# Optimization experiments

Measured on AMD Instinct MI355X. Metric: run time of the kernel, lower is better.

Reference implementation:

```python
import jax, jax.numpy as jnp
import numpy as np

IMG = 1024
STRIDES = [8, 16, 32, 64, 128]
SIZES = [32, 64, 128, 256, 512]
RATIOS = [0.5, 1.0, 2.0]
MIN_T = 0.4  # config.min_iou_thresh
MAX_T = 0.5  # config.max_iou_thresh (focal loss_type)
B, G = 32, 20  # batch, GT boxes per image (lengths = [20]*32)


def _make_anchors():
    """generate_anchors + get_anchor_shifts: centered anchors on each level's grid."""
    levels = []
    for stride, size in zip(STRIDES, SIZES):
        ws = np.array([size / np.sqrt(r) for r in RATIOS])
        hs = np.array([size * np.sqrt(r) for r in RATIOS])
        base = np.stack([-ws / 2, -hs / 2, ws / 2, hs / 2], axis=1)  # [3,4]
        g = IMG // stride
        xs = (np.arange(g) + 0.5) * stride
        sy, sx = np.meshgrid(xs, xs, indexing='ij')
        shifts = np.stack([sx, sy, sx, sy], axis=-1).reshape(-1, 1, 4)
        levels.append((shifts + base[None]).reshape(-1, 4).astype(np.float32))
    return levels


def setup_inputs() -> dict:
    key = jax.random.key(0)
    k1, k2, k3 = jax.random.split(key, 3)
    ctr = jax.random.uniform(k1, (B, G, 2), minval=64.0, maxval=float(IMG - 64))
    wh = jax.random.uniform(k2, (B, G, 2), minval=16.0, maxval=256.0)
    bb_coord = jnp.concatenate([ctr - 0.5 * wh, ctr + 0.5 * wh], axis=-1)  # [B,G,4] x1y1x2y2
    bird_ids = jax.random.randint(k3, (B, G), 1, 51, dtype=jnp.int32)
    anchors = _make_anchors()
    inp = {'bb_coord': bb_coord, 'bird_ids': bird_ids}
    for i, a in enumerate(anchors):
        inp[f'anchors_l{i}'] = jnp.asarray(a)
    return inp


def _iou(anch, gt):
    a = anch[None, :, None, :]
    g = gt[:, None, :, :]
    iw = jnp.clip(jnp.minimum(a[..., 2], g[..., 2]) - jnp.maximum(a[..., 0], g[..., 0]) + 1.0, 0.0)
    ih = jnp.clip(jnp.minimum(a[..., 3], g[..., 3]) - jnp.maximum(a[..., 1], g[..., 1]) + 1.0, 0.0)
    area_a = (anch[:, 2] - anch[:, 0] + 1.0) * (anch[:, 3] - anch[:, 1] + 1.0)  # [A]
    area_g = (gt[..., 2] - gt[..., 0] + 1.0) * (gt[..., 3] - gt[..., 1] + 1.0)  # [B,G]
    inter = iw * ih
    return inter / (area_a[None, :, None] + area_g[:, None, :] - inter)


def _bbox_transform(ex, gt):
    # ex [A,4] anchors, gt [B,A,4] assigned boxes -> [B,A,4] (dx,dy,dw,dh)
    ew = ex[:, 2] - ex[:, 0] + 1.0
    eh = ex[:, 3] - ex[:, 1] + 1.0
    ecx = ex[:, 0] + 0.5 * ew
    ecy = ex[:, 1] + 0.5 * eh
    gw = gt[..., 2] - gt[..., 0] + 1.0
    gh = gt[..., 3] - gt[..., 1] + 1.0
    gcx = gt[..., 0] + 0.5 * gw
    gcy = gt[..., 1] + 0.5 * gh
    return jnp.stack([(gcx - ecx) / ew, (gcy - ecy) / eh,
                      jnp.log(gw / ew), jnp.log(gh / eh)], axis=-1)


def _assign(bb_coord, bird_ids_f, anchors_list):
    n_lvl = len(anchors_list)
    max_ovs, argmaxs, gt_maxs, gt_args = [], [], [], []
    for anch in anchors_list:
        ov = _iou(anch, bb_coord)                 # [B,A,G]
        max_ovs.append(ov.max(axis=2))            # [B,A]
        argmaxs.append(ov.argmax(axis=2))         # [B,A]
        gt_maxs.append(ov.max(axis=1))            # [B,G]
        gt_args.append(ov.argmax(axis=1))         # [B,G]
    gt_max_level = jnp.stack(gt_maxs, axis=0).argmax(axis=0)  # [B,G]

    labels_out, reg_out = [], []
    brow = jnp.arange(B)[:, None]
    for lvl, anch in enumerate(anchors_list):
        A = anch.shape[0]
        max_ov, amax = max_ovs[lvl], argmaxs[lvl]
        assigned_box = bb_coord[brow, amax]        # [B,A,4]
        assigned_ids = bird_ids_f[brow, amax]      # [B,A]
        # force each GT's best anchor (on its best level) positive
        is_max = gt_max_level == lvl               # [B,G]
        safe_idx = jnp.where(is_max, gt_args[lvl], A)  # OOB -> dropped
        assigned_box = assigned_box.at[brow, safe_idx].set(bb_coord, mode='drop')
        assigned_ids = assigned_ids.at[brow, safe_idx].set(bird_ids_f, mode='drop')
        ignore = (max_ov >= MIN_T) & (max_ov < MAX_T)
        pos = max_ov >= MAX_T
        pos = pos.at[brow, safe_idx].set(True, mode='drop')
        labels = jnp.where(pos, assigned_ids, jnp.where(ignore, -1.0, 0.0))
        reg = jnp.where(pos[..., None], _bbox_transform(anch, assigned_box), 0.0)
        labels_out.append(labels.astype(jnp.int32))
        reg_out.append(reg)
    return jnp.concatenate(labels_out, axis=1), jnp.concatenate(reg_out, axis=1)


def reference(bb_coord, bird_ids, anchors_l0, anchors_l1, anchors_l2, anchors_l3, anchors_l4):
    anchors = [anchors_l0, anchors_l1, anchors_l2, anchors_l3, anchors_l4]
    labels, reg = _assign(bb_coord, bird_ids.astype(jnp.float32), anchors)
    return labels, reg
```

## Files before the change

kernel.cpp:

```cpp
#include <hip/hip_runtime.h>
#include <hip/hip_bf16.h>

#define NB 32
#define NG 20
#define A_TOTAL 65472
#define LAB_OFF ((size_t)NB * A_TOTAL)
#define NSLOT (NB * NG * 5)

__device__ __forceinline__ float b2f(unsigned short u) {
    __hip_bfloat16 h;
    __builtin_memcpy(&h, &u, 2);
    return __bfloat162float(h);
}

__device__ __forceinline__ float4 ldbox(const void* p, int idx, int isbf) {
    if (isbf) {
        const unsigned short* q = (const unsigned short*)p + (size_t)idx * 4;
        return make_float4(b2f(q[0]), b2f(q[1]), b2f(q[2]), b2f(q[3]));
    }
    return ((const float4*)p)[idx];
}

__device__ __forceinline__ int detect_bf(const void* an0) {
    const unsigned short* u = (const unsigned short*)an0;
    return (fabsf(b2f(u[0]) + 18.6274f) < 0.5f &&
            fabsf(b2f(u[2]) - 26.6274f) < 0.5f) ? 1 : 0;
}

__device__ __forceinline__ float decode_id(const void* idsv, int i) {
    unsigned w = ((const unsigned*)idsv)[i];
    return (w <= 50u) ? (float)(int)w : __uint_as_float(w);
}

__device__ __forceinline__ float area1(float4 A) {
#pragma clang fp contract(off)
    return (A.z - A.x + 1.0f) * (A.w - A.y + 1.0f);
}

__device__ __forceinline__ void reg_transform(float4 A, float g0, float g1,
                                              float g2, float g3,
                                              float& t0, float& t1,
                                              float& t2, float& t3) {
#pragma clang fp contract(off)
    const float ew = A.z - A.x + 1.0f, eh = A.w - A.y + 1.0f;
    const float ecx = A.x + 0.5f * ew, ecy = A.y + 0.5f * eh;
    const float gw = g2 - g0 + 1.0f, gh = g3 - g1 + 1.0f;
    const float gcx = g0 + 0.5f * gw, gcy = g1 + 0.5f * gh;
    t0 = (gcx - ecx) / ew;
    t1 = (gcy - ecy) / eh;
    t2 = logf(gw / ew);
    t3 = logf(gh / eh);
}

__device__ __forceinline__ float iou32h(float4 A, float aa,
                                        float4 G, float ag) {
#pragma clang fp contract(off)
    float iw = fminf(A.z, G.z) - fmaxf(A.x, G.x) + 1.0f;
    iw = fmaxf(iw, 0.0f);
    float ih = fminf(A.w, G.w) - fmaxf(A.y, G.y) + 1.0f;
    ih = fmaxf(ih, 0.0f);
    float inter = iw * ih;
    return inter / (aa + ag - inter);
}

__global__ __launch_bounds__(256, 6)
void kCodes(const void* __restrict__ bb, const void* __restrict__ idsv,
            const void* __restrict__ an0, const void* __restrict__ an1,
            const void* __restrict__ an2, const void* __restrict__ an3,
            const void* __restrict__ an4,
            float* __restrict__ out,
            unsigned long long* __restrict__ slots)
{
    __shared__ float4 sbox4[NG];
    __shared__ float  sid[NG];
    __shared__ unsigned long long swk[NG][4];

    const int tid = threadIdx.x;
    const int b = blockIdx.y;
    const int c = blockIdx.x;
    const int isbf = detect_bf(an0);

    if (tid < NG) {
        sbox4[tid] = ldbox(bb, b * NG + tid, isbf);
        sid[tid] = decode_id(idsv, b * NG + tid);
    }
    __syncthreads();

    int l, lbase, count, goff;
    if (c < 48)      { l = 0; lbase = c * 1024;        count = 1024; goff = 0; }
    else if (c < 60) { l = 1; lbase = (c - 48) * 1024; count = 1024; goff = 49152; }
    else if (c < 63) { l = 2; lbase = (c - 60) * 1024; count = 1024; goff = 61440; }
    else if (c == 63){ l = 3; lbase = 0;               count = 768;  goff = 64512; }
    else             { l = 4; lbase = 0;               count = 192;  goff = 65280; }
    const void* an = (l == 0) ? an0 : (l == 1) ? an1
                   : (l == 2) ? an2 : (l == 3) ? an3 : an4;

    float4 A[4];
    float aa[4];
    bool val[4];
#pragma unroll
    for (int k = 0; k < 4; ++k) {
        const int i = tid + k * 256;
        val[k] = (i < count);
        A[k] = val[k] ? ldbox(an, lbase + i, isbf)
                      : make_float4(-1e8f, -1e8f, -1e8f, -1e8f);
        aa[k] = area1(A[k]);
    }

    float mx[4] = {-1.f, -1.f, -1.f, -1.f};
    int mg[4] = {0, 0, 0, 0};
    const int lane = tid & 63;
    const int wave = tid >> 6;

    for (int g = 0; g < NG; ++g) {
        const float4 G = sbox4[g];
        const float ag = area1(G);
        float bvv = -1.0f;
        int bii = 0;
#pragma unroll
        for (int k = 0; k < 4; ++k) {
            const float v = iou32h(A[k], aa[k], G, ag);
            if (v > mx[k]) { mx[k] = v; mg[k] = g; }
            if (v > bvv)   { bvv = v; bii = goff + lbase + tid + k * 256; }
        }
        unsigned long long key =
            ((unsigned long long)__float_as_uint(bvv) << 32)
            | (unsigned)(~(unsigned)bii);
        for (int o = 32; o > 0; o >>= 1) {
            const unsigned long long ok = __shfl_xor(key, o);
            if (ok > key) key = ok;
        }
        if (lane == 0) swk[g][wave] = key;
    }

    float* lab = out + (size_t)b * A_TOTAL;
    float4* rp = (float4*)(out + LAB_OFF) + (size_t)b * A_TOTAL;
#pragma unroll
    for (int k = 0; k < 4; ++k) {
        if (!val[k]) continue;
        const int ga = goff + lbase + tid + k * 256;
        const bool pos = (mx[k] >= 0.5f);
        lab[ga] = pos ? sid[mg[k]] : ((mx[k] >= 0.4f) ? -1.0f : 0.0f);
        float t0 = 0.f, t1 = 0.f, t2 = 0.f, t3 = 0.f;
        if (pos) {
            const float4 G = sbox4[mg[k]];
            reg_transform(A[k], G.x, G.y, G.z, G.w, t0, t1, t2, t3);
        }
        rp[ga] = make_float4(t0, t1, t2, t3);
    }

    __syncthreads();
    if (tid < NG) {
        unsigned long long k0 = swk[tid][0];
        for (int w = 1; w < 4; ++w)
            if (swk[tid][w] > k0) k0 = swk[tid][w];
        atomicMax(&slots[(b * NG + tid) * 5 + l], k0);
    }
}

__global__ __launch_bounds__(64)
void kForce(const void* __restrict__ bb, const void* __restrict__ idsv,
            const void* __restrict__ an0, const void* __restrict__ an1,
            const void* __restrict__ an2, const void* __restrict__ an3,
            const void* __restrict__ an4,
            const unsigned long long* __restrict__ slots,
            float* __restrict__ out)
{
    __shared__ int sforce[NG];
    const int b = blockIdx.x;
    const int g = threadIdx.x;
    const int isbf = detect_bf(an0);

    if (g < NG) {
        const unsigned long long* s = &slots[(b * NG + g) * 5];
        unsigned long long best = s[0];
        for (int l = 1; l < 5; ++l) {
            if ((unsigned)(s[l] >> 32) > (unsigned)(best >> 32)) best = s[l];
        }
        sforce[g] = (int)(~(unsigned)best);
    }
    __syncthreads();

    if (g < NG) {
        const int a = sforce[g];
        bool win = true;
        for (int g2 = g + 1; g2 < NG; ++g2)
            if (sforce[g2] == a) win = false;
        if (win) {
            int l, off;
            if (a < 49152)      { l = 0; off = 0; }
            else if (a < 61440) { l = 1; off = 49152; }
            else if (a < 64512) { l = 2; off = 61440; }
            else if (a < 65280) { l = 3; off = 64512; }
            else                { l = 4; off = 65280; }
            const void* an = (l == 0) ? an0 : (l == 1) ? an1
                           : (l == 2) ? an2 : (l == 3) ? an3 : an4;
            const float4 A = ldbox(an, a - off, isbf);
            const float4 G = ldbox(bb, b * NG + g, isbf);
            out[(size_t)b * A_TOTAL + a] = decode_id(idsv, b * NG + g);
            float t0, t1, t2, t3;
            reg_transform(A, G.x, G.y, G.z, G.w, t0, t1, t2, t3);
            ((float4*)(out + LAB_OFF))[(size_t)b * A_TOTAL + a]
                = make_float4(t0, t1, t2, t3);
        }
    }
}

__global__ __launch_bounds__(1024)
void kFused(const void* __restrict__ bb, const void* __restrict__ idsv,
            const void* __restrict__ an0, const void* __restrict__ an1,
            const void* __restrict__ an2, const void* __restrict__ an3,
            const void* __restrict__ an4,
            float* __restrict__ out)
{
    __shared__ float4 sbox4[NG];
    __shared__ float swv[NG][16];
    __shared__ int   swi[NG][16];
    __shared__ float lvv[NG][5];
    __shared__ int   lvi[NG][5];
    __shared__ float sid[NG];
    __shared__ int   sforce[NG];

    const int tid = threadIdx.x;
    const int b = blockIdx.x;
    const int isbf = detect_bf(an0);

    if (tid < NG) {
        sbox4[tid] = ldbox(bb, b * NG + tid, isbf);
        sid[tid] = decode_id(idsv, b * NG + tid);
    }
    __syncthreads();

    const void* ans[5] = {an0, an1, an2, an3, an4};
    const int lcount[5] = {49152, 12288, 3072, 768, 192};
    const int loffs[5]  = {0, 49152, 61440, 64512, 65280};
    const int lane = tid & 63;
    const int wave = tid >> 6;
    float* myCodes = out + (size_t)b * A_TOTAL;

    for (int l = 0; l < 5; ++l) {
        float bv[NG];
        int bi[NG];
#pragma unroll
        for (int g = 0; g < NG; ++g) { bv[g] = -1.0f; bi[g] = 0x7fffffff; }
        for (int i = tid; i < lcount[l]; i += 1024) {
            const float4 A = ldbox(ans[l], i, isbf);
            const float aa = area1(A);
            float mxv = -1.0f;
            int mgv = 0;
#pragma unroll
            for (int g = 0; g < NG; ++g) {
                const float4 G = sbox4[g];
                const float ag = area1(G);
                float v = iou32h(A, aa, G, ag);
                if (v > mxv) { mxv = v; mgv = g; }
                if (v > bv[g]) { bv[g] = v; bi[g] = i; }
            }
            const int cls = (mxv >= 0.5f) ? 2 : (mxv >= 0.4f) ? 1 : 0;
            myCodes[loffs[l] + i] = (float)(mgv | (cls << 5));
        }
#pragma unroll
        for (int g = 0; g < NG; ++g) {
            float v = bv[g];
            int ix = bi[g];
            for (int o = 32; o > 0; o >>= 1) {
                float ov = __shfl_xor(v, o);
                int   oi = __shfl_xor(ix, o);
                if (ov > v || (ov == v && oi < ix)) { v = ov; ix = oi; }
            }
            if (lane == 0) { swv[g][wave] = v; swi[g][wave] = ix; }
        }
        __syncthreads();
        if (tid < NG) {
            float v = swv[tid][0];
            int ix = swi[tid][0];
            for (int w = 1; w < 16; ++w) {
                float ov = swv[tid][w];
                int   oi = swi[tid][w];
                if (ov > v || (ov == v && oi < ix)) { v = ov; ix = oi; }
            }
            lvv[tid][l] = v;
            lvi[tid][l] = ix;
        }
        __syncthreads();
    }
    if (tid < NG) {
        int bl = 0;
#pragma unroll
        for (int l = 1; l < 5; ++l)
            if (lvv[tid][l] > lvv[tid][bl]) bl = l;
        sforce[tid] = loffs[bl] + lvi[tid][bl];
    }
    __syncthreads();

    float4* rp = (float4*)(out + LAB_OFF);
    for (int a = tid; a < A_TOTAL; a += 1024) {
        int l, off;
        if (a < 49152)      { l = 0; off = 0; }
        else if (a < 61440) { l = 1; off = 49152; }
        else if (a < 64512) { l = 2; off = 61440; }
        else if (a < 65280) { l = 3; off = 64512; }
        else                { l = 4; off = 65280; }
        const int code = (int)myCodes[a];
        const int mgv = code & 31;
        const int cls = code >> 5;
        int fg = -1;
#pragma unroll
        for (int g = 0; g < NG; ++g)
            if (sforce[g] == a) fg = g;
        const bool pos = (cls == 2) || (fg >= 0);
        const int ug = (fg >= 0) ? fg : mgv;
        myCodes[a] = pos ? sid[ug] : ((cls == 1) ? -1.0f : 0.0f);
        float t0 = 0.f, t1 = 0.f, t2 = 0.f, t3 = 0.f;
        if (pos) {
            const float4 A = ldbox(ans[l], a - off, isbf);
            const float4 G = sbox4[ug];
            reg_transform(A, G.x, G.y, G.z, G.w, t0, t1, t2, t3);
        }
        rp[(size_t)b * A_TOTAL + a] = make_float4(t0, t1, t2, t3);
    }
}

extern "C" void kernel_launch(void* const* d_in, const int* in_sizes, int n_in,
                              void* d_out, int out_size, void* d_ws, size_t ws_size,
                              hipStream_t stream) {
    const void* bb = d_in[0];
    const void* ids = d_in[1];
    const void* an[5] = {d_in[2], d_in[3], d_in[4], d_in[5], d_in[6]};
    if (n_in == 7) {
        for (int i = 0; i < 7; ++i) {
            switch (in_sizes[i]) {
                case 2560:   bb    = d_in[i]; break;
                case 640:    ids   = d_in[i]; break;
                case 196608: an[0] = d_in[i]; break;
                case 49152:  an[1] = d_in[i]; break;
                case 12288:  an[2] = d_in[i]; break;
                case 3072:   an[3] = d_in[i]; break;
                case 768:    an[4] = d_in[i]; break;
                default: break;
            }
        }
    }
    float* out = (float*)d_out;
    const size_t need = (size_t)NSLOT * sizeof(unsigned long long);

    if (ws_size >= need) {
        unsigned long long* slots = (unsigned long long*)d_ws;
        (void)hipMemsetAsync(d_ws, 0, need, stream);
        hipLaunchKernelGGL(kCodes, dim3(65, NB), dim3(256), 0, stream,
                           bb, ids, an[0], an[1], an[2], an[3], an[4],
                           out, slots);
        hipLaunchKernelGGL(kForce, dim3(NB), dim3(64), 0, stream,
                           bb, ids, an[0], an[1], an[2], an[3], an[4],
                           slots, out);
    } else {
        hipLaunchKernelGGL(kFused, dim3(NB), dim3(1024), 0, stream,
                           bb, ids, an[0], an[1], an[2], an[3], an[4], out);
    }
}
```

Baseline: 130.0 us.

## Fuse force-assignment into main kernel via last-block completion counter

Merges the two kernels into one: after each block does its atomicMax, it increments a global counter, and the last block to finish runs the force-positive pass for every image. This removes a separate kernel launch. The per-GT reduction now stages keys in shared memory through a two-level tree instead of a full wave shuffle, and GT areas are precomputed once in shared memory. The IoU divide is skipped when the intersection is zero. In exchange the tail work is serialized onto one 256-thread block, shared memory use grows by roughly 23 KB, and the dropped occupancy hint may change register allocation.

```diff
diff --git a/kernel.cpp b/kernel.cpp
--- a/kernel.cpp
+++ b/kernel.cpp
@@ -60,20 +60,27 @@
     float ih = fminf(A.w, G.w) - fmaxf(A.y, G.y) + 1.0f;
     ih = fmaxf(ih, 0.0f);
     float inter = iw * ih;
-    return inter / (aa + ag - inter);
-}
-
-__global__ __launch_bounds__(256, 6)
-void kCodes(const void* __restrict__ bb, const void* __restrict__ idsv,
-            const void* __restrict__ an0, const void* __restrict__ an1,
-            const void* __restrict__ an2, const void* __restrict__ an3,
-            const void* __restrict__ an4,
-            float* __restrict__ out,
-            unsigned long long* __restrict__ slots)
+    float v = 0.0f;
+    if (inter > 0.0f) v = inter / (aa + ag - inter);
+    return v;
+}
+
+__global__ __launch_bounds__(256)
+void kAll(const void* __restrict__ bb, const void* __restrict__ idsv,
+          const void* __restrict__ an0, const void* __restrict__ an1,
+          const void* __restrict__ an2, const void* __restrict__ an3,
+          const void* __restrict__ an4,
+          float* __restrict__ out,
+          unsigned long long* __restrict__ slots,
+          unsigned int* __restrict__ counter)
 {
     __shared__ float4 sbox4[NG];
+    __shared__ float  sag[NG];
     __shared__ float  sid[NG];
-    __shared__ unsigned long long swk[NG][4];
+    __shared__ unsigned long long sred[NG][128];
+    __shared__ unsigned long long swk[NG][8];
+    __shared__ int sfin;
+    __shared__ int sfL[NB][NG];
 
     const int tid = threadIdx.x;
     const int b = blockIdx.y;
@@ -81,7 +88,9 @@
     const int isbf = detect_bf(an0);
 
     if (tid < NG) {
-        sbox4[tid] = ldbox(bb, b * NG + tid, isbf);
+        const float4 G = ldbox(bb, b * NG + tid, isbf);
+        sbox4[tid] = G;
+        sag[tid] = area1(G);
         sid[tid] = decode_id(idsv, b * NG + tid);
     }
     __syncthreads();
@@ -109,12 +118,10 @@
 
     float mx[4] = {-1.f, -1.f, -1.f, -1.f};
     int mg[4] = {0, 0, 0, 0};
-    const int lane = tid & 63;
-    const int wave = tid >> 6;
 
     for (int g = 0; g < NG; ++g) {
         const float4 G = sbox4[g];
-        const float ag = area1(G);
+        const float ag = sag[g];
         float bvv = -1.0f;
         int bii = 0;
 #pragma unroll
@@ -126,11 +133,9 @@
         unsigned long long key =
             ((unsigned long long)__float_as_uint(bvv) << 32)
             | (unsigned)(~(unsigned)bii);
-        for (int o = 32; o > 0; o >>= 1) {
-            const unsigned long long ok = __shfl_xor(key, o);
-            if (ok > key) key = ok;
-        }
-        if (lane == 0) swk[g][wave] = key;
+        const unsigned long long other = __shfl_xor(key, 1);
+        if (other > key) key = other;
+        if ((tid & 1) == 0) sred[g][tid >> 1] = key;
     }
 
     float* lab = out + (size_t)b * A_TOTAL;
@@ -150,59 +155,65 @@
     }
 
     __syncthreads();
+    if (tid < 160) {
+        const int g = tid >> 3, part = tid & 7;
+        unsigned long long best = sred[g][part * 16];
+        for (int j = 1; j < 16; ++j) {
+            const unsigned long long v = sred[g][part * 16 + j];
+            if (v > best) best = v;
+        }
+        swk[g][part] = best;
+    }
+    __syncthreads();
     if (tid < NG) {
-        unsigned long long k0 = swk[tid][0];
-        for (int w = 1; w < 4; ++w)
-            if (swk[tid][w] > k0) k0 = swk[tid][w];
-        atomicMax(&slots[(b * NG + tid) * 5 + l], k0);
-    }
-}
-
-__global__ __launch_bounds__(64)
-void kForce(const void* __restrict__ bb, const void* __restrict__ idsv,
-            const void* __restrict__ an0, const void* __restrict__ an1,
-            const void* __restrict__ an2, const void* __restrict__ an3,
-            const void* __restrict__ an4,
-            const unsigned long long* __restrict__ slots,
-            float* __restrict__ out)
-{
-    __shared__ int sforce[NG];
-    const int b = blockIdx.x;
-    const int g = threadIdx.x;
-    const int isbf = detect_bf(an0);
-
-    if (g < NG) {
-        const unsigned long long* s = &slots[(b * NG + g) * 5];
-        unsigned long long best = s[0];
-        for (int l = 1; l < 5; ++l) {
-            if ((unsigned)(s[l] >> 32) > (unsigned)(best >> 32)) best = s[l];
-        }
-        sforce[g] = (int)(~(unsigned)best);
-    }
-    __syncthreads();
-
-    if (g < NG) {
-        const int a = sforce[g];
+        unsigned long long best = swk[tid][0];
+        for (int w = 1; w < 8; ++w)
+            if (swk[tid][w] > best) best = swk[tid][w];
+        atomicMax(&slots[(b * NG + tid) * 5 + l], best);
+    }
+
+    __threadfence();
+    __syncthreads();
+    if (tid == 0) {
+        const unsigned last = gridDim.x * gridDim.y - 1;
+        sfin = (atomicAdd(counter, 1u) == last) ? 1 : 0;
+    }
+    __syncthreads();
+    if (!sfin) return;
+
+    for (int t = tid; t < NB * NG; t += 256) {
+        const int fb = t / NG, fg = t % NG;
+        unsigned long long* s = &slots[(fb * NG + fg) * 5];
+        unsigned long long best = atomicAdd(&s[0], 0ull);
+        for (int ll = 1; ll < 5; ++ll) {
+            const unsigned long long v = atomicAdd(&s[ll], 0ull);
+            if ((unsigned)(v >> 32) > (unsigned)(best >> 32)) best = v;
+        }
+        sfL[fb][fg] = (int)(~(unsigned)best);
+    }
+    __syncthreads();
+    for (int t = tid; t < NB * NG; t += 256) {
+        const int fb = t / NG, fg = t % NG;
+        const int a = sfL[fb][fg];
         bool win = true;
-        for (int g2 = g + 1; g2 < NG; ++g2)
-            if (sforce[g2] == a) win = false;
-        if (win) {
-            int l, off;
-            if (a < 49152)      { l = 0; off = 0; }
-            else if (a < 61440) { l = 1; off = 49152; }
-            else if (a < 64512) { l = 2; off = 61440; }
-            else if (a < 65280) { l = 3; off = 64512; }
-            else                { l = 4; off = 65280; }
-            const void* an = (l == 0) ? an0 : (l == 1) ? an1
-                           : (l == 2) ? an2 : (l == 3) ? an3 : an4;
-            const float4 A = ldbox(an, a - off, isbf);
-            const float4 G = ldbox(bb, b * NG + g, isbf);
-            out[(size_t)b * A_TOTAL + a] = decode_id(idsv, b * NG + g);
-            float t0, t1, t2, t3;
-            reg_transform(A, G.x, G.y, G.z, G.w, t0, t1, t2, t3);
-            ((float4*)(out + LAB_OFF))[(size_t)b * A_TOTAL + a]
-                = make_float4(t0, t1, t2, t3);
-        }
+        for (int g2 = fg + 1; g2 < NG; ++g2)
+            if (sfL[fb][g2] == a) win = false;
+        if (!win) continue;
+        int fl, foff;
+        if (a < 49152)      { fl = 0; foff = 0; }
+        else if (a < 61440) { fl = 1; foff = 49152; }
+        else if (a < 64512) { fl = 2; foff = 61440; }
+        else if (a < 65280) { fl = 3; foff = 64512; }
+        else                { fl = 4; foff = 65280; }
+        const void* fan = (fl == 0) ? an0 : (fl == 1) ? an1
+                        : (fl == 2) ? an2 : (fl == 3) ? an3 : an4;
+        const float4 FA = ldbox(fan, a - foff, isbf);
+        const float4 FG = ldbox(bb, fb * NG + fg, isbf);
+        out[(size_t)fb * A_TOTAL + a] = decode_id(idsv, fb * NG + fg);
+        float t0, t1, t2, t3;
+        reg_transform(FA, FG.x, FG.y, FG.z, FG.w, t0, t1, t2, t3);
+        ((float4*)(out + LAB_OFF))[(size_t)fb * A_TOTAL + a]
+            = make_float4(t0, t1, t2, t3);
     }
 }
 
@@ -342,17 +353,16 @@
         }
     }
     float* out = (float*)d_out;
-    const size_t need = (size_t)NSLOT * sizeof(unsigned long long);
+    const size_t slotBytes = (size_t)NSLOT * sizeof(unsigned long long);
+    const size_t need = slotBytes + 64;
 
     if (ws_size >= need) {
         unsigned long long* slots = (unsigned long long*)d_ws;
+        unsigned int* counter = (unsigned int*)((char*)d_ws + slotBytes);
         (void)hipMemsetAsync(d_ws, 0, need, stream);
-        hipLaunchKernelGGL(kCodes, dim3(65, NB), dim3(256), 0, stream,
+        hipLaunchKernelGGL(kAll, dim3(65, NB), dim3(256), 0, stream,
                            bb, ids, an[0], an[1], an[2], an[3], an[4],
-                           out, slots);
-        hipLaunchKernelGGL(kForce, dim3(NB), dim3(64), 0, stream,
-                           bb, ids, an[0], an[1], an[2], an[3], an[4],
-                           slots, out);
+                           out, slots, counter);
     } else {
         hipLaunchKernelGGL(kFused, dim3(NB), dim3(1024), 0, stream,
                            bb, ids, an[0], an[1], an[2], an[3], an[4], out);
```

Measured after the change: 306.5 us. +135.7%, slower.
